# Kernel optimization log

Measured on AMD Instinct MI355X. Metric: run time of the kernel, lower is better.

Reference implementation:

```python
import math
import jax, jax.numpy as jnp
import numpy as np

B, C, H, W = 8, 512, 32, 32
NUM_HEADS = 8
HEAD_DIM = C // NUM_HEADS


def setup_inputs() -> dict:
    key = jax.random.key(0)
    ks = jax.random.split(key, 5)
    scale = 1.0 / math.sqrt(C)
    return {
        "x": jax.random.normal(ks[0], (B, C, H, W), dtype=jnp.float32),
        "Wq": jax.random.normal(ks[1], (C, C), dtype=jnp.float32) * scale,
        "bq": jnp.zeros((C,), dtype=jnp.float32),
        "Wk": jax.random.normal(ks[2], (C, C), dtype=jnp.float32) * scale,
        "bk": jnp.zeros((C,), dtype=jnp.float32),
        "Wv": jax.random.normal(ks[3], (C, C), dtype=jnp.float32) * scale,
        "bv": jnp.zeros((C,), dtype=jnp.float32),
        "Wo": jax.random.normal(ks[4], (C, C), dtype=jnp.float32) * scale,
        "bo": jnp.zeros((C,), dtype=jnp.float32),
    }


def reference(x, Wq, bq, Wk, bk, Wv, bv, Wo, bo):
    b, c, h, w = x.shape
    t = h * w
    # (B,C,H,W) -> (B,T,C) token sequence
    xt = x.reshape(b, c, t).transpose(0, 2, 1)
    Q = xt @ Wq + bq
    K = xt @ Wk + bk
    V = xt @ Wv + bv
    # (B,T,C) -> (B,nh,T,hd)
    def split_heads(z):
        return z.reshape(b, t, NUM_HEADS, HEAD_DIM).transpose(0, 2, 1, 3)
    Qh, Kh, Vh = split_heads(Q), split_heads(K), split_heads(V)
    S = jnp.einsum("bhqd,bhkd->bhqk", Qh, Kh) / math.sqrt(HEAD_DIM)
    A = jax.nn.softmax(S, axis=-1)  # dropout p=0.0 -> identity
    Y = jnp.einsum("bhqk,bhkd->bhqd", A, Vh)
    Y = Y.transpose(0, 2, 1, 3).reshape(b, t, c)
    O = Y @ Wo + bo
    out = xt + O
    return out.transpose(0, 2, 1).reshape(b, c, h, w)
```

## Files before the change

### kernel.cpp

```cpp
#include <hip/hip_runtime.h>
#include <hip/hip_bf16.h>

#define B_  8
#define C_  512
#define T_  1024
#define NH_ 8
#define HD_ 64

#define QSCALE 0.1803368801111243f

using short8 = __attribute__((ext_vector_type(8))) short;
using f32x4  = __attribute__((ext_vector_type(4))) float;
using f32x16 = __attribute__((ext_vector_type(16))) float;
using us4    = __attribute__((ext_vector_type(4))) unsigned short;

__device__ __forceinline__ unsigned short f2bf(float f) {
    unsigned u = __builtin_bit_cast(unsigned, f);
    u += 0x7fff + ((u >> 16) & 1);
    return (unsigned short)(u >> 16);
}
__device__ __forceinline__ unsigned pack2bf(float lo, float hi) {
    __hip_bfloat162 h = __float22bfloat162_rn(float2{lo, hi});
    unsigned u;
    __builtin_memcpy(&u, &h, 4);
    return u;
}

__device__ __forceinline__ void gload_lds16(const ushort* g, ushort* l) {
    __builtin_amdgcn_global_load_lds(
        (const __attribute__((address_space(1))) void*)g,
        (__attribute__((address_space(3))) void*)l, 16, 0, 0);
}

template <int N>
__device__ __forceinline__ void wait_vmcnt() {
    asm volatile("s_waitcnt vmcnt(%0)" ::"n"(N) : "memory");
    __builtin_amdgcn_sched_barrier(0);
}
__device__ __forceinline__ void barrier_raw() {
    __builtin_amdgcn_sched_barrier(0);
    __builtin_amdgcn_s_barrier();
}

__global__ __launch_bounds__(256) void k_prep(const float* __restrict__ x,
                                              const float* __restrict__ Wq,
                                              const float* __restrict__ Wk,
                                              const float* __restrict__ Wv,
                                              const float* __restrict__ Wo,
                                              ushort* __restrict__ xt,
                                              ushort* __restrict__ Wqkvt,
                                              ushort* __restrict__ Wot) {
    __shared__ float tile[32][33];
    int L = blockIdx.x;
    int tx = threadIdx.x & 31, ty = threadIdx.x >> 5;
    if (L < 4096) {
        int b = L >> 9, rem = L & 511;
        int t0 = (rem & 31) * 32, c0 = (rem >> 5) * 32;
#pragma unroll
        for (int i = 0; i < 4; i++)
            tile[ty + i * 8][tx] = x[((size_t)b * C_ + c0 + ty + i * 8) * T_ + t0 + tx];
        __syncthreads();
#pragma unroll
        for (int i = 0; i < 4; i++)
            xt[((size_t)b * T_ + t0 + ty + i * 8) * C_ + c0 + tx] = f2bf(tile[tx][ty + i * 8]);
    } else {
        int LL = L - 4096;
        int m = LL >> 8, rem = LL & 255;
        int k0 = (rem & 15) * 32, n0 = (rem >> 4) * 32;
        const float* W = (m == 0) ? Wq : (m == 1) ? Wk : (m == 2) ? Wv : Wo;
        ushort* dst = (m < 3) ? (Wqkvt + (size_t)m * C_ * C_) : Wot;
        float scale = (m == 0) ? QSCALE : 1.0f;
#pragma unroll
        for (int i = 0; i < 4; i++)
            tile[ty + i * 8][tx] = W[(size_t)(k0 + ty + i * 8) * C_ + n0 + tx];
        __syncthreads();
#pragma unroll
        for (int i = 0; i < 4; i++)
            dst[(size_t)(n0 + ty + i * 8) * C_ + k0 + tx] = f2bf(tile[tx][ty + i * 8] * scale);
    }
}

__device__ __forceinline__ void gemm_core(const ushort* __restrict__ A,
                                          const ushort* __restrict__ Bt,
                                          int row0, int col0, int tid,
                                          ushort (*As)[8192], ushort (*Bs)[8192],
                                          f32x4 acc[4][4]) {
    f32x4 zero = {0.f, 0.f, 0.f, 0.f};
#pragma unroll
    for (int i = 0; i < 4; i++)
#pragma unroll
        for (int j = 0; j < 4; j++) acc[i][j] = zero;
    int lane = tid & 63, w = tid >> 6;
    int ql = lane & 15, g = lane >> 4;
    int wm = (w >> 1) * 64, wn = (w & 1) * 64;
    int srow = lane >> 3;
    int scol8 = (lane & 7) ^ (srow & 7);

#pragma unroll
    for (int i = 0; i < 4; i++) {
        int c = w * 4 + i;
        int r = c * 8 + srow;
        gload_lds16(A + (size_t)(row0 + r) * C_ + scol8 * 8, As[0] + c * 512);
        gload_lds16(Bt + (size_t)(col0 + r) * C_ + scol8 * 8, Bs[0] + c * 512);
    }

#pragma unroll
    for (int kt = 0; kt < 8; kt++) {
        int cur = kt & 1;
        if (kt < 7) {
            int k0 = (kt + 1) * 64;
#pragma unroll
            for (int i = 0; i < 4; i++) {
                int c = w * 4 + i;
                int r = c * 8 + srow;
                gload_lds16(A + (size_t)(row0 + r) * C_ + k0 + scol8 * 8, As[cur ^ 1] + c * 512);
                gload_lds16(Bt + (size_t)(col0 + r) * C_ + k0 + scol8 * 8, Bs[cur ^ 1] + c * 512);
            }
            wait_vmcnt<8>();
        } else {
            wait_vmcnt<0>();
        }
        barrier_raw();
        const ushort* Ac = As[cur];
        const ushort* Bc = Bs[cur];
        __builtin_amdgcn_s_setprio(1);
#pragma unroll
        for (int s = 0; s < 2; s++) {
            short8 a[4], b[4];
            int cs = ((4 * s + g) ^ (ql & 7)) * 8;
#pragma unroll
            for (int mt = 0; mt < 4; mt++)
                a[mt] = *(const short8*)(Ac + (wm + mt * 16 + ql) * 64 + cs);
#pragma unroll
            for (int nt = 0; nt < 4; nt++)
                b[nt] = *(const short8*)(Bc + (wn + nt * 16 + ql) * 64 + cs);
#pragma unroll
            for (int mt = 0; mt < 4; mt++)
#pragma unroll
                for (int nt = 0; nt < 4; nt++)
                    acc[mt][nt] = __builtin_amdgcn_mfma_f32_16x16x32_bf16(
                        a[mt], b[nt], acc[mt][nt], 0, 0, 0);
        }
        __builtin_amdgcn_s_setprio(0);
        barrier_raw();
    }
}

__global__ __launch_bounds__(256) void k_qkv(const ushort* __restrict__ xt,
                                             const ushort* __restrict__ Wqkvt,
                                             const float* __restrict__ bq,
                                             const float* __restrict__ bk,
                                             const float* __restrict__ bv,
                                             ushort* __restrict__ Qh,
                                             ushort* __restrict__ Kh,
                                             ushort* __restrict__ Vt) {
    __shared__ __align__(16) ushort As[2][8192];
    __shared__ __align__(16) ushort Bs[2][8192];
    f32x4 acc[4][4];
    int tid = threadIdx.x;
    int L = blockIdx.x;
    int n = L >> 3, xcd = L & 7;
    int row0 = (xcd * 8 + (n & 7)) * 128;
    int col0 = (n >> 3) * 128;
    gemm_core(xt, Wqkvt, row0, col0, tid, As, Bs, acc);
    int lane = tid & 63, w = tid >> 6;
    int wm = (w >> 1) * 64, wn = (w & 1) * 64;
    int which = col0 >> 9;
    const float* bias = (which == 0) ? bq : (which == 1) ? bk : bv;
    float bscale = (which == 0) ? QSCALE : 1.0f;
#pragma unroll
    for (int mt = 0; mt < 4; mt++) {
        int grow0 = row0 + wm + mt * 16 + ((lane >> 4) << 2);
        int b = grow0 >> 10, t = grow0 & 1023;
#pragma unroll
        for (int nt = 0; nt < 4; nt++) {
            int gcol = col0 + wn + nt * 16 + (lane & 15);
            int hc = gcol & 511;
            float bsv = bias[hc] * bscale;
            int h = hc >> 6, d = hc & 63;
            if (which == 2) {
                us4 pk;
#pragma unroll
                for (int r = 0; r < 4; r++) pk[r] = f2bf(acc[mt][nt][r] + bsv);
                *(us4*)(Vt + ((size_t)(b * NH_ + h) * HD_ + d) * T_ + t) = pk;
            } else {
                ushort* dst = (which == 0) ? Qh : Kh;
#pragma unroll
                for (int r = 0; r < 4; r++)
                    dst[((size_t)(b * NH_ + h) * T_ + t + r) * HD_ + d] =
                        f2bf(acc[mt][nt][r] + bsv);
            }
        }
    }
}

__global__ __launch_bounds__(256) void k_attn(const ushort* __restrict__ Qh,
                                              const ushort* __restrict__ Kh,
                                              const ushort* __restrict__ Vt,
                                              ushort* __restrict__ Y) {
    __shared__ __align__(16) ushort Ks[2][64 * 64];
    __shared__ __align__(16) ushort Vs[2][64 * 64];
    int tid = threadIdx.x, lane = tid & 63, w = tid >> 6;
    int hi = lane >> 5, l31 = lane & 31, l7 = lane & 7;
    int bh = blockIdx.x & 63, q0 = (blockIdx.x >> 6) * 128;
    int b = bh >> 3, h = bh & 7;
    int srow = lane >> 3;
    int scol8 = l7 ^ (srow & 7);
    const ushort* Kbase = Kh + (size_t)bh * T_ * HD_;
    const ushort* Vbase = Vt + (size_t)bh * HD_ * T_;

    short8 qa[4];
#pragma unroll
    for (int s = 0; s < 4; s++)
        qa[s] = *(const short8*)(Qh + ((size_t)bh * T_ + q0 + w * 32 + l31) * HD_ +
                                 s * 16 + hi * 8);

    f32x16 o0, o1;
#pragma unroll
    for (int i = 0; i < 16; i++) { o0[i] = 0.f; o1[i] = 0.f; }
    float lsum = 0.f;

#pragma unroll
    for (int i = 0; i < 2; i++) {
        int c = w * 2 + i;
        int r = c * 8 + srow;
        gload_lds16(Kbase + (size_t)r * HD_ + scol8 * 8, Ks[0] + c * 512);
        gload_lds16(Vbase + (size_t)r * T_ + scol8 * 8, Vs[0] + c * 512);
    }

    for (int t = 0; t < 16; t++) {
        int cur = t & 1;
        const ushort* Kc = Ks[cur];
        const ushort* Vc = Vs[cur];
        if (t < 15) {
            int kv0 = (t + 1) * 64;
#pragma unroll
            for (int i = 0; i < 2; i++) {
                int c = w * 2 + i;
                int r = c * 8 + srow;
                gload_lds16(Kbase + (size_t)(kv0 + r) * HD_ + scol8 * 8, Ks[cur ^ 1] + c * 512);
                gload_lds16(Vbase + (size_t)r * T_ + kv0 + scol8 * 8, Vs[cur ^ 1] + c * 512);
            }
            wait_vmcnt<4>();
        } else {
            wait_vmcnt<0>();
        }
        barrier_raw();

        f32x16 sT0, sT1;
#pragma unroll
        for (int i = 0; i < 16; i++) { sT0[i] = 0.f; sT1[i] = 0.f; }
        __builtin_amdgcn_s_setprio(1);
#pragma unroll
        for (int s = 0; s < 4; s++) {
            int cs = ((2 * s + hi) ^ l7) * 8;
            short8 ka0 = *(const short8*)(Kc + l31 * 64 + cs);
            short8 ka1 = *(const short8*)(Kc + (32 + l31) * 64 + cs);
            sT0 = __builtin_amdgcn_mfma_f32_32x32x16_bf16(ka0, qa[s], sT0, 0, 0, 0);
            sT1 = __builtin_amdgcn_mfma_f32_32x32x16_bf16(ka1, qa[s], sT1, 0, 0, 0);
        }
        __builtin_amdgcn_s_setprio(0);

        unsigned pkv0[8], pkv1[8];
        float ts = 0.f;
#pragma unroll
        for (int i = 0; i < 8; i++) {
            float a0 = __builtin_amdgcn_exp2f(sT0[2 * i]);
            float a1 = __builtin_amdgcn_exp2f(sT0[2 * i + 1]);
            float b0 = __builtin_amdgcn_exp2f(sT1[2 * i]);
            float b1 = __builtin_amdgcn_exp2f(sT1[2 * i + 1]);
            pkv0[i] = pack2bf(a0, a1);
            pkv1[i] = pack2bf(b0, b1);
            ts += (a0 + a1) + (b0 + b1);
        }
        lsum += ts;

        __builtin_amdgcn_s_setprio(1);
#pragma unroll
        for (int t4 = 0; t4 < 4; t4++) {
            const int h2 = t4 & 1;
            unsigned c0, c1, c2v, c3v;
            if (t4 < 2) {
                c0 = pkv0[4 * h2 + 0]; c2v = pkv0[4 * h2 + 2];
                c1 = pkv0[4 * h2 + 1]; c3v = pkv0[4 * h2 + 3];
            } else {
                c0 = pkv1[4 * h2 + 0]; c2v = pkv1[4 * h2 + 2];
                c1 = pkv1[4 * h2 + 1]; c3v = pkv1[4 * h2 + 3];
            }
            asm("v_permlane32_swap_b32 %0, %1" : "+v"(c0), "+v"(c2v));
            asm("v_permlane32_swap_b32 %0, %1" : "+v"(c1), "+v"(c3v));
            unsigned au[4] = {c0, c1, c2v, c3v};
            short8 pa;
            __builtin_memcpy(&pa, au, 16);
            int cs = ((2 * t4 + hi) ^ l7) * 8;
            short8 vb0 = *(const short8*)(Vc + l31 * 64 + cs);
            short8 vb1 = *(const short8*)(Vc + (32 + l31) * 64 + cs);
            o0 = __builtin_amdgcn_mfma_f32_32x32x16_bf16(pa, vb0, o0, 0, 0, 0);
            o1 = __builtin_amdgcn_mfma_f32_32x32x16_bf16(pa, vb1, o1, 0, 0, 0);
        }
        __builtin_amdgcn_s_setprio(0);
        barrier_raw();
    }

    float linv = 1.0f / (lsum + __shfl_xor(lsum, 32));
#pragma unroll
    for (int r = 0; r < 16; r++) {
        int qr = (r & 3) + 8 * (r >> 2) + 4 * hi;
        float li = __shfl(linv, qr);
        int trow = q0 + w * 32 + qr;
        size_t base = ((size_t)b * T_ + trow) * C_ + h * HD_;
        Y[base + l31] = f2bf(o0[r] * li);
        Y[base + 32 + l31] = f2bf(o1[r] * li);
    }
}

__global__ __launch_bounds__(256) void k_oproj(const ushort* __restrict__ Y,
                                               const ushort* __restrict__ Wot,
                                               const float* __restrict__ bo,
                                               const float* __restrict__ x,
                                               float* __restrict__ out) {
    __shared__ __align__(16) ushort As[2][8192];
    __shared__ __align__(16) ushort Bs[2][8192];
    f32x4 acc[4][4];
    int tid = threadIdx.x;
    int L = blockIdx.x;
    int n = L >> 3, xcd = L & 7;
    int row0 = (xcd * 8 + (n & 7)) * 128;
    int col0 = (n >> 3) * 128;
    gemm_core(Y, Wot, row0, col0, tid, As, Bs, acc);
    int lane = tid & 63, w = tid >> 6;
    int wm = (w >> 1) * 64, wn = (w & 1) * 64;
#pragma unroll
    for (int mt = 0; mt < 4; mt++) {
        int grow0 = row0 + wm + mt * 16 + ((lane >> 4) << 2);
        int b = grow0 >> 10, t = grow0 & 1023;
#pragma unroll
        for (int nt = 0; nt < 4; nt++) {
            int c = col0 + wn + nt * 16 + (lane & 15);
            float bsv = bo[c];
            size_t off = ((size_t)b * C_ + c) * T_ + t;
            float4 xv = *(const float4*)(x + off);
            float4 ov;
            ov.x = acc[mt][nt][0] + xv.x + bsv;
            ov.y = acc[mt][nt][1] + xv.y + bsv;
            ov.z = acc[mt][nt][2] + xv.z + bsv;
            ov.w = acc[mt][nt][3] + xv.w + bsv;
            *(float4*)(out + off) = ov;
        }
    }
}

extern "C" void kernel_launch(void* const* d_in, const int* in_sizes, int n_in,
                              void* d_out, int out_size, void* d_ws, size_t ws_size,
                              hipStream_t stream) {
    const float* x  = (const float*)d_in[0];
    const float* Wq = (const float*)d_in[1];
    const float* bq = (const float*)d_in[2];
    const float* Wk = (const float*)d_in[3];
    const float* bk = (const float*)d_in[4];
    const float* Wv = (const float*)d_in[5];
    const float* bv = (const float*)d_in[6];
    const float* Wo = (const float*)d_in[7];
    const float* bo = (const float*)d_in[8];
    float* out = (float*)d_out;

    char* ws = (char*)d_ws;
    ushort* xt    = (ushort*)(ws + 0);
    ushort* Wqkvt = (ushort*)(ws + 8388608);
    ushort* Wot   = (ushort*)(ws + 9961472);
    ushort* Qh    = (ushort*)(ws + 10485760);
    ushort* Kh    = (ushort*)(ws + 18874368);
    ushort* Vt    = (ushort*)(ws + 27262976);
    ushort* Yw    = xt;

    k_prep<<<dim3(5120), 256, 0, stream>>>(x, Wq, Wk, Wv, Wo, xt, Wqkvt, Wot);
    k_qkv<<<dim3(768), 256, 0, stream>>>(xt, Wqkvt, bq, bk, bv, Qh, Kh, Vt);
    k_attn<<<dim3(512), 256, 0, stream>>>(Qh, Kh, Vt, Yw);
    k_oproj<<<dim3(256), 256, 0, stream>>>(Yw, Wot, bo, x, out);
}
```

Measured before the change: 77.30 us.

## Stage QKV epilogue through LDS for vector stores; compute softmax row sums via MFMA

The QKV GEMM epilogue now writes tiles into swizzled shared memory and then issues 16-byte coalesced global stores for Q/K and for the transposed V, replacing scattered 2-byte and 8-byte stores. In attention, the row-sum of exponentials is computed with an extra MFMA against a ones vector instead of VALU adds, and the K/V buffers are merged into one LDS array with precomputed offsets, a fully unrolled tile loop and no zero-init of the score accumulators. The costs are an extra LDS round trip and barrier in the epilogue, and one extra MFMA per PV step. The row sums are now built from the bf16-rounded probabilities rather than the fp32 values.

```diff
diff --git a/kernel.cpp b/kernel.cpp
--- a/kernel.cpp
+++ b/kernel.cpp
@@ -164,32 +164,70 @@
     int col0 = (n >> 3) * 128;
     gemm_core(xt, Wqkvt, row0, col0, tid, As, Bs, acc);
     int lane = tid & 63, w = tid >> 6;
+    int ql = lane & 15, g = lane >> 4;
     int wm = (w >> 1) * 64, wn = (w & 1) * 64;
     int which = col0 >> 9;
     const float* bias = (which == 0) ? bq : (which == 1) ? bk : bv;
     float bscale = (which == 0) ? QSCALE : 1.0f;
-#pragma unroll
-    for (int mt = 0; mt < 4; mt++) {
-        int grow0 = row0 + wm + mt * 16 + ((lane >> 4) << 2);
-        int b = grow0 >> 10, t = grow0 & 1023;
-#pragma unroll
-        for (int nt = 0; nt < 4; nt++) {
-            int gcol = col0 + wn + nt * 16 + (lane & 15);
-            int hc = gcol & 511;
-            float bsv = bias[hc] * bscale;
-            int h = hc >> 6, d = hc & 63;
-            if (which == 2) {
+    ushort* Lt = &As[0][0];
+
+    if (which < 3 && which != 2) {
+        ushort* dst = (which == 0) ? Qh : Kh;
+#pragma unroll
+        for (int mt = 0; mt < 4; mt++)
+#pragma unroll
+            for (int nt = 0; nt < 4; nt++) {
+                int col = wn + nt * 16 + ql;
+                float bsv = bias[(col0 + col) & 511] * bscale;
+#pragma unroll
+                for (int r = 0; r < 4; r++) {
+                    int row = wm + mt * 16 + 4 * g + r;
+                    int sw = col ^ ((row & 7) << 3);
+                    Lt[row * 128 + sw] = f2bf(acc[mt][nt][r] + bsv);
+                }
+            }
+        __syncthreads();
+#pragma unroll
+        for (int i = 0; i < 8; i++) {
+            int task = w * 512 + i * 64 + lane;
+            int row = task >> 4, gran = task & 15;
+            int sg = gran ^ (row & 7);
+            short8 vle = *(const short8*)(Lt + row * 128 + sg * 8);
+            int gcol = col0 + gran * 8;
+            int hc = gcol & 511, h = hc >> 6, d = hc & 63;
+            int grow = row0 + row, b = grow >> 10, t = grow & 1023;
+            *(short8*)(dst + ((size_t)(b * NH_ + h) * T_ + t) * HD_ + d) = vle;
+        }
+    } else {
+#pragma unroll
+        for (int mt = 0; mt < 4; mt++)
+#pragma unroll
+            for (int nt = 0; nt < 4; nt++) {
+                int col = wn + nt * 16 + ql;
+                float bsv = bias[(col0 + col) & 511] * bscale;
+                int rowb = wm + mt * 16 + 4 * g;
+                int swz = (rowb >> 2) ^ (col & 31);
                 us4 pk;
 #pragma unroll
                 for (int r = 0; r < 4; r++) pk[r] = f2bf(acc[mt][nt][r] + bsv);
-                *(us4*)(Vt + ((size_t)(b * NH_ + h) * HD_ + d) * T_ + t) = pk;
-            } else {
-                ushort* dst = (which == 0) ? Qh : Kh;
-#pragma unroll
-                for (int r = 0; r < 4; r++)
-                    dst[((size_t)(b * NH_ + h) * T_ + t + r) * HD_ + d] =
-                        f2bf(acc[mt][nt][r] + bsv);
+                *(us4*)(Lt + col * 128 + swz * 4) = pk;
             }
+        __syncthreads();
+#pragma unroll
+        for (int i = 0; i < 8; i++) {
+            int task = w * 512 + i * 64 + lane;
+            int colr = task >> 4, gran = task & 15;
+            int g4a = (2 * gran) ^ (colr & 31);
+            int g4b = (2 * gran + 1) ^ (colr & 31);
+            us4 lo = *(const us4*)(Lt + colr * 128 + g4a * 4);
+            us4 hi4 = *(const us4*)(Lt + colr * 128 + g4b * 4);
+            us4 arr[2] = {lo, hi4};
+            short8 vle;
+            __builtin_memcpy(&vle, arr, 16);
+            int gcol = col0 + colr;
+            int hc = gcol & 511, h = hc >> 6, d = hc & 63;
+            int grow = row0 + gran * 8, b = grow >> 10, t = grow & 1023;
+            *(short8*)(Vt + ((size_t)(b * NH_ + h) * HD_ + d) * T_ + t) = vle;
         }
     }
 }
@@ -198,8 +236,7 @@
                                               const ushort* __restrict__ Kh,
                                               const ushort* __restrict__ Vt,
                                               ushort* __restrict__ Y) {
-    __shared__ __align__(16) ushort Ks[2][64 * 64];
-    __shared__ __align__(16) ushort Vs[2][64 * 64];
+    __shared__ __align__(16) ushort KV[4][4096];
     int tid = threadIdx.x, lane = tid & 63, w = tid >> 6;
     int hi = lane >> 5, l31 = lane & 31, l7 = lane & 7;
     int bh = blockIdx.x & 63, q0 = (blockIdx.x >> 6) * 128;
@@ -208,6 +245,7 @@
     int scol8 = l7 ^ (srow & 7);
     const ushort* Kbase = Kh + (size_t)bh * T_ * HD_;
     const ushort* Vbase = Vt + (size_t)bh * HD_ * T_;
+    const ushort* kv = &KV[0][0];
 
     short8 qa[4];
 #pragma unroll
@@ -215,31 +253,43 @@
         qa[s] = *(const short8*)(Qh + ((size_t)bh * T_ + q0 + w * 32 + l31) * HD_ +
                                  s * 16 + hi * 8);
 
-    f32x16 o0, o1;
-#pragma unroll
-    for (int i = 0; i < 16; i++) { o0[i] = 0.f; o1[i] = 0.f; }
-    float lsum = 0.f;
+    int fofs[4];
+#pragma unroll
+    for (int s = 0; s < 4; s++) fofs[s] = ((2 * s + hi) ^ l7) * 8;
+    int rowlo = l31 * 64;
+
+    short8 ones;
+    {
+        short ov = (l31 == 0) ? (short)0x3F80 : (short)0;
+#pragma unroll
+        for (int j = 0; j < 8; j++) ones[j] = ov;
+    }
+
+    f32x16 o0, o1, o5, z16;
+#pragma unroll
+    for (int i = 0; i < 16; i++) { o0[i] = 0.f; o1[i] = 0.f; o5[i] = 0.f; z16[i] = 0.f; }
 
 #pragma unroll
     for (int i = 0; i < 2; i++) {
         int c = w * 2 + i;
         int r = c * 8 + srow;
-        gload_lds16(Kbase + (size_t)r * HD_ + scol8 * 8, Ks[0] + c * 512);
-        gload_lds16(Vbase + (size_t)r * T_ + scol8 * 8, Vs[0] + c * 512);
-    }
-
+        gload_lds16(Kbase + (size_t)r * HD_ + scol8 * 8, &KV[0][0] + c * 512);
+        gload_lds16(Vbase + (size_t)r * T_ + scol8 * 8, &KV[2][0] + c * 512);
+    }
+
+#pragma unroll
     for (int t = 0; t < 16; t++) {
-        int cur = t & 1;
-        const ushort* Kc = Ks[cur];
-        const ushort* Vc = Vs[cur];
+        const int cur = t & 1;
         if (t < 15) {
             int kv0 = (t + 1) * 64;
 #pragma unroll
             for (int i = 0; i < 2; i++) {
                 int c = w * 2 + i;
                 int r = c * 8 + srow;
-                gload_lds16(Kbase + (size_t)(kv0 + r) * HD_ + scol8 * 8, Ks[cur ^ 1] + c * 512);
-                gload_lds16(Vbase + (size_t)r * T_ + kv0 + scol8 * 8, Vs[cur ^ 1] + c * 512);
+                gload_lds16(Kbase + (size_t)(kv0 + r) * HD_ + scol8 * 8,
+                            &KV[cur ^ 1][0] + c * 512);
+                gload_lds16(Vbase + (size_t)r * T_ + kv0 + scol8 * 8,
+                            &KV[2 + (cur ^ 1)][0] + c * 512);
             }
             wait_vmcnt<4>();
         } else {
@@ -248,32 +298,30 @@
         barrier_raw();
 
         f32x16 sT0, sT1;
-#pragma unroll
-        for (int i = 0; i < 16; i++) { sT0[i] = 0.f; sT1[i] = 0.f; }
         __builtin_amdgcn_s_setprio(1);
-#pragma unroll
-        for (int s = 0; s < 4; s++) {
-            int cs = ((2 * s + hi) ^ l7) * 8;
-            short8 ka0 = *(const short8*)(Kc + l31 * 64 + cs);
-            short8 ka1 = *(const short8*)(Kc + (32 + l31) * 64 + cs);
+        {
+            short8 ka0 = *(const short8*)(kv + cur * 4096 + rowlo + fofs[0]);
+            short8 ka1 = *(const short8*)(kv + cur * 4096 + 2048 + rowlo + fofs[0]);
+            sT0 = __builtin_amdgcn_mfma_f32_32x32x16_bf16(ka0, qa[0], z16, 0, 0, 0);
+            sT1 = __builtin_amdgcn_mfma_f32_32x32x16_bf16(ka1, qa[0], z16, 0, 0, 0);
+        }
+#pragma unroll
+        for (int s = 1; s < 4; s++) {
+            short8 ka0 = *(const short8*)(kv + cur * 4096 + rowlo + fofs[s]);
+            short8 ka1 = *(const short8*)(kv + cur * 4096 + 2048 + rowlo + fofs[s]);
             sT0 = __builtin_amdgcn_mfma_f32_32x32x16_bf16(ka0, qa[s], sT0, 0, 0, 0);
             sT1 = __builtin_amdgcn_mfma_f32_32x32x16_bf16(ka1, qa[s], sT1, 0, 0, 0);
         }
         __builtin_amdgcn_s_setprio(0);
 
         unsigned pkv0[8], pkv1[8];
-        float ts = 0.f;
 #pragma unroll
         for (int i = 0; i < 8; i++) {
-            float a0 = __builtin_amdgcn_exp2f(sT0[2 * i]);
-            float a1 = __builtin_amdgcn_exp2f(sT0[2 * i + 1]);
-            float b0 = __builtin_amdgcn_exp2f(sT1[2 * i]);
-            float b1 = __builtin_amdgcn_exp2f(sT1[2 * i + 1]);
-            pkv0[i] = pack2bf(a0, a1);
-            pkv1[i] = pack2bf(b0, b1);
-            ts += (a0 + a1) + (b0 + b1);
-        }
-        lsum += ts;
+            pkv0[i] = pack2bf(__builtin_amdgcn_exp2f(sT0[2 * i]),
+                              __builtin_amdgcn_exp2f(sT0[2 * i + 1]));
+            pkv1[i] = pack2bf(__builtin_amdgcn_exp2f(sT1[2 * i]),
+                              __builtin_amdgcn_exp2f(sT1[2 * i + 1]));
+        }
 
         __builtin_amdgcn_s_setprio(1);
 #pragma unroll
@@ -292,21 +340,20 @@
             unsigned au[4] = {c0, c1, c2v, c3v};
             short8 pa;
             __builtin_memcpy(&pa, au, 16);
-            int cs = ((2 * t4 + hi) ^ l7) * 8;
-            short8 vb0 = *(const short8*)(Vc + l31 * 64 + cs);
-            short8 vb1 = *(const short8*)(Vc + (32 + l31) * 64 + cs);
+            short8 vb0 = *(const short8*)(kv + (2 + cur) * 4096 + rowlo + fofs[t4]);
+            short8 vb1 = *(const short8*)(kv + (2 + cur) * 4096 + 2048 + rowlo + fofs[t4]);
             o0 = __builtin_amdgcn_mfma_f32_32x32x16_bf16(pa, vb0, o0, 0, 0, 0);
             o1 = __builtin_amdgcn_mfma_f32_32x32x16_bf16(pa, vb1, o1, 0, 0, 0);
+            o5 = __builtin_amdgcn_mfma_f32_32x32x16_bf16(pa, ones, o5, 0, 0, 0);
         }
         __builtin_amdgcn_s_setprio(0);
         barrier_raw();
     }
 
-    float linv = 1.0f / (lsum + __shfl_xor(lsum, 32));
 #pragma unroll
     for (int r = 0; r < 16; r++) {
+        float li = 1.0f / __shfl(o5[r], hi * 32);
         int qr = (r & 3) + 8 * (r >> 2) + 4 * hi;
-        float li = __shfl(linv, qr);
         int trow = q0 + w * 32 + qr;
         size_t base = ((size_t)b * T_ + trow) * C_ + h * HD_;
         Y[base + l31] = f2bf(o0[r] * li);
```

New measurement: 73.09 us. 5.4% less time.
